# Kernel optimization log

Measured on AMD Instinct MI355X. Metric: run time of the kernel, lower is better.

The kernel has to match this reference:

```python
import jax, jax.numpy as jnp
import numpy as np

B, T, C = 64, 200, 53
EMB, HID, AH, OUT = 64, 128, 128, 2
C2 = C * C
D1 = round(0.05 * C2)   # 140
D2 = round(0.5 * C2)    # 1404
BN_EPS = 1e-5


def setup_inputs() -> dict:
    key = jax.random.key(0)
    ks = jax.random.split(key, 32)
    def rn(k, shape, s=0.1):
        return (jax.random.normal(k, shape) * s).astype(jnp.float32)
    return {
        "x": rn(ks[0], (B, T, C), 1.0),
        # single shared Linear(1, EMB) embedding
        "emb_w": rn(ks[1], (EMB,)), "emb_b": rn(ks[2], (EMB,)),
        # GRU cell (weights stored [in, 3*HID], gate order r,z,n like torch)
        "w_ih": rn(ks[3], (EMB, 3 * HID)), "w_hh": rn(ks[4], (HID, 3 * HID)),
        "b_ih": rn(ks[5], (3 * HID,)), "b_hh": rn(ks[6], (3 * HID,)),
        # self-attention projections
        "q_w": rn(ks[7], (HID, AH)), "q_b": rn(ks[8], (AH,)),
        "k_w": rn(ks[9], (HID, AH)), "k_b": rn(ks[10], (AH,)),
        "v_w": rn(ks[11], (HID, HID)), "v_b": rn(ks[12], (HID,)),
        "gate_b": rn(ks[13], (C, C), 1.0),  # Gate.bias = randn(C, C)
        # gta_embed + BatchNorm1d + gta_attend
        "ge_w": rn(ks[14], (C2, D1)), "ge_b": rn(ks[15], (D1,)),
        "bn_g": jnp.ones((D1,), jnp.float32), "bn_b": jnp.zeros((D1,), jnp.float32),
        "ga_w1": rn(ks[16], (D1, D2)), "ga_b1": rn(ks[17], (D2,)),
        "ga_w2": rn(ks[18], (D2, 1)), "ga_b2": rn(ks[19], (1,)),
        # classifier MLP
        "c_w1": rn(ks[20], (C2, C2 // 2)), "c_b1": rn(ks[21], (C2 // 2,)),
        "c_w2": rn(ks[22], (C2 // 2, C2 // 4)), "c_b2": rn(ks[23], (C2 // 4,)),
        "c_w3": rn(ks[24], (C2 // 4, OUT)), "c_b3": rn(ks[25], (OUT,)),
    }


def _forward(x, emb_w, emb_b, w_ih, w_hh, b_ih, b_hh, q_w, q_b, k_w, k_b,
             v_w, v_b, gate_b, ge_w, ge_b, bn_g, bn_b, ga_w1, ga_b1, ga_w2,
             ga_b2, c_w1, c_b1, c_w2, c_b2, c_w3, c_b3):
    # Linear(1, EMB) applied per scalar: [B,T,C] -> [B,C,T,EMB]
    e = x.transpose(0, 2, 1)[..., None] * emb_w + emb_b
    xs = jnp.moveaxis(e, 2, 0)  # [T, B, C, EMB]

    def step(h, x_t):  # h: [B,C,HID], x_t: [B,C,EMB]
        gi = x_t @ w_ih + b_ih
        gh = h @ w_hh + b_hh
        i_r, i_z, i_n = jnp.split(gi, 3, axis=-1)
        h_r, h_z, h_n = jnp.split(gh, 3, axis=-1)
        r = jax.nn.sigmoid(i_r + h_r)
        z = jax.nn.sigmoid(i_z + h_z)
        n = jnp.tanh(i_n + r * h_n)
        h_new = (1 - z) * n + z * h
        # SVD-normalized self-attention across components
        q = h_new @ q_w + q_b
        k = h_new @ k_w + k_b
        v = h_new @ v_w + v_b
        scores = jnp.tanh(jnp.einsum('bif,bjf->bij', q, k))  # use_tan='before'
        sv = jnp.linalg.svd(scores, compute_uv=False)         # [B,C]
        ev = jax.lax.stop_gradient(jnp.max(jnp.abs(sv), axis=1))[:, None, None]
        scores = scores / ev
        attn = scores * jax.nn.sigmoid(jnp.abs(scores) + gate_b)  # Gate
        h_out = jnp.einsum('bij,bjf->bif', attn, v)
        return h_out, attn

    h0 = jnp.zeros((B, C, HID), x.dtype)
    _, attns = jax.lax.scan(step, h0, xs)      # [T,B,C,C]
    align = jnp.moveaxis(attns, 0, 1)          # [B,T,C,C]

    # gta_attention over time axis
    ai = align.reshape(B, T, C2)
    xr = (ai * ai.mean(axis=1, keepdims=True)).reshape(B * T, C2)
    xe = xr @ ge_w + ge_b
    mu = xe.mean(axis=0)
    var = xe.var(axis=0)  # biased, matches torch BN training-mode normalization
    xn = jax.nn.relu((xe - mu) / jnp.sqrt(var + BN_EPS) * bn_g + bn_b)
    a = jax.nn.relu(xn @ ga_w1 + ga_b1) @ ga_w2 + ga_b2  # [B*T,1]
    w = jax.nn.softmax(a.reshape(B, T), axis=1)
    dnc = (ai * w[..., None]).sum(axis=1)      # [B, C2]

    # classifier (Dropout1d is identity at inference)
    h1 = jax.nn.relu(dnc @ c_w1 + c_b1)
    h2 = jax.nn.relu(h1 @ c_w2 + c_b2)
    logits = h2 @ c_w3 + c_b3
    return logits, dnc.reshape(B, C, C), align


def reference(x, emb_w, emb_b, w_ih, w_hh, b_ih, b_hh, q_w, q_b, k_w, k_b,
              v_w, v_b, gate_b, ge_w, ge_b, bn_g, bn_b, ga_w1, ga_b1, ga_w2,
              ga_b2, c_w1, c_b1, c_w2, c_b2, c_w3, c_b3):
    return _forward(x, emb_w, emb_b, w_ih, w_hh, b_ih, b_hh, q_w, q_b, k_w,
                    k_b, v_w, v_b, gate_b, ge_w, ge_b, bn_g, bn_b, ga_w1,
                    ga_b1, ga_w2, ga_b2, c_w1, c_b1, c_w2, c_b2, c_w3, c_b3)
```

## Files before the change

kernel.cpp:

```cpp
#include <hip/hip_runtime.h>

#define NT 1024

__device__ __forceinline__ float fast_sigmoid(float x) { return 1.f/(1.f + __expf(-x)); }
__device__ __forceinline__ float fast_tanh(float x) {
  float t = __expf(-2.f*fabsf(x));
  float y = (1.f - t)/(1.f + t);
  return copysignf(y, x);
}
__device__ __forceinline__ void acc4(float& a, float4 u, float4 v) {
  a = fmaf(u.x, v.x, a); a = fmaf(u.y, v.y, a); a = fmaf(u.z, v.z, a); a = fmaf(u.w, v.w, a);
}
#define FMA4(A_, S_, V_) do { (A_).x = fmaf((S_),(V_).x,(A_).x); (A_).y = fmaf((S_),(V_).y,(A_).y); \
                              (A_).z = fmaf((S_),(V_).z,(A_).z); (A_).w = fmaf((S_),(V_).w,(A_).w); } while(0)

struct alignas(16) SmemScan {
  float h[56][132];
  float z[56][132];
  float v[56][132];
  float S[56][60];
  float G0[56][60];
  float GA[56][60];
  float GB[56][60];
  float u384[384], v00[384];
  float xt[56];
  float pv[56], y1[56], y2[56];
  int   gmax[9];
  float sc_ev;
};

__global__ void prep_whT(const float* __restrict__ w_hh, const float* __restrict__ b_hh,
                         float* __restrict__ WhT) {
  int idx = blockIdx.x*256 + threadIdx.x;
  if (idx >= 384*132) return;
  int g = idx/132, c = idx - g*132;
  float v = 0.f;
  if (c < 128) v = w_hh[c*384 + g];
  else if (c == 128) v = b_hh[g];
  WhT[idx] = v;
}

__global__ void prep_wT(const float* __restrict__ q_w, const float* __restrict__ q_b,
                        const float* __restrict__ k_w, const float* __restrict__ k_b,
                        const float* __restrict__ v_w, const float* __restrict__ v_b,
                        float* __restrict__ WT) {
  int idx = blockIdx.x*256 + threadIdx.x;
  if (idx >= 257*132) return;
  int u = idx/132, c = idx - u*132;
  float val = 0.f;
  if (u < 129) {
    if (c <= 128) {
      const float* qa = (c < 128) ? (q_w + c*128) : q_b;
      const float* kb = (u < 128) ? (k_w + u*128) : k_b;
      float s = 0.f;
      for (int d = 0; d < 128; ++d) s = fmaf(qa[d], kb[d], s);
      val = s;
    }
  } else {
    int f = u - 129;
    if (c < 128) val = v_w[c*128 + f];
    else if (c == 128) val = v_b[f];
  }
  WT[idx] = val;
}

__global__ void __launch_bounds__(1024, 4)
scan_kernel(const float* __restrict__ x, const float* __restrict__ emb_w,
            const float* __restrict__ emb_b, const float* __restrict__ w_ih,
            const float* __restrict__ b_ih, const float* __restrict__ WhT,
            const float* __restrict__ WT, const float* __restrict__ gate_b,
            float* __restrict__ out_align)
{
  extern __shared__ char smem_raw[];
  SmemScan& sm = *reinterpret_cast<SmemScan*>(smem_raw);
  const int b = blockIdx.x;
  const int tid = threadIdx.x;
  const int wv = tid >> 6;
  const int lane = tid & 63;

  for (int j = tid; j < 384; j += NT) {
    float su = 0.f, sv = 0.f;
    for (int m = 0; m < 64; ++m) {
      float w = w_ih[m*384 + j];
      su = fmaf(emb_w[m], w, su);
      sv = fmaf(emb_b[m], w, sv);
    }
    sm.u384[j] = su;
    sm.v00[j]  = sv + b_ih[j];
  }
  for (int idx = tid; idx < 56*132; idx += NT) {
    int r = idx/132, c = idx - r*132;
    float hv = (c == 128 && r < 53) ? 1.f : 0.f;
    sm.h[r][c] = hv; sm.z[r][c] = 0.f; sm.v[r][c] = 0.f;
  }
  for (int idx = tid; idx < 56*60; idx += NT) {
    int r = idx/60, c = idx - r*60;
    sm.S[r][c] = 0.f; sm.G0[r][c] = 0.f; sm.GA[r][c] = 0.f; sm.GB[r][c] = 0.f;
  }
  __syncthreads();

  const int f  = tid & 127;
  const int c0 = tid >> 7;
  int  cix[7]; bool cok[7];
  #pragma unroll
  for (int i = 0; i < 7; ++i) { int cc = c0 + 8*i; cok[i] = (cc < 53); cix[i] = cok[i] ? cc : 52; }

  const float* wh0 = WhT + (size_t)f*132;
  const float* wh1 = WhT + (size_t)(128+f)*132;
  const float* wh2 = WhT + (size_t)(256+f)*132;
  const int colA = 2*f, colB = colA + 1;
  const float* wtA = WT + (size_t)colA*132;
  const float* wtB = WT + (size_t)colB*132;

  for (int t = 0; t < 200; ++t) {
    if (tid < 53) sm.xt[tid] = x[(b*200 + t)*53 + tid];
    __syncthreads();

    float a0[7], a1[7], a2[7];
    #pragma unroll
    for (int i = 0; i < 7; ++i) { a0[i] = 0.f; a1[i] = 0.f; a2[i] = 0.f; }
    for (int q = 0; q < 33; ++q) {
      float4 w0 = *(const float4*)(wh0 + 4*q);
      float4 w1 = *(const float4*)(wh1 + 4*q);
      float4 w2 = *(const float4*)(wh2 + 4*q);
      #pragma unroll
      for (int i = 0; i < 7; ++i) {
        float4 hv = *(const float4*)&sm.h[cix[i]][4*q];
        acc4(a0[i], hv, w0); acc4(a1[i], hv, w1); acc4(a2[i], hv, w2);
      }
    }
    float hnew[7];
    {
      float uf0 = sm.u384[f], uf1 = sm.u384[128+f], uf2 = sm.u384[256+f];
      float v0f0 = sm.v00[f], v0f1 = sm.v00[128+f], v0f2 = sm.v00[256+f];
      #pragma unroll
      for (int i = 0; i < 7; ++i) {
        float xs = sm.xt[cix[i]];
        float r = fast_sigmoid(fmaf(xs, uf0, v0f0) + a0[i]);
        float z = fast_sigmoid(fmaf(xs, uf1, v0f1) + a1[i]);
        float n = fast_tanh(fmaf(xs, uf2, v0f2) + fmaf(r, a2[i], 0.f));
        hnew[i] = (1.f - z)*n + z*sm.h[cix[i]][f];
      }
    }
    __syncthreads();
    #pragma unroll
    for (int i = 0; i < 7; ++i) if (cok[i]) sm.h[cix[i]][f] = hnew[i];
    __syncthreads();

    {
      float aA[7], aB[7];
      #pragma unroll
      for (int i = 0; i < 7; ++i) { aA[i] = 0.f; aB[i] = 0.f; }
      for (int q = 0; q < 33; ++q) {
        float4 wa = *(const float4*)(wtA + 4*q);
        float4 wb = *(const float4*)(wtB + 4*q);
        #pragma unroll
        for (int i = 0; i < 7; ++i) {
          float4 hv = *(const float4*)&sm.h[cix[i]][4*q];
          acc4(aA[i], hv, wa); acc4(aB[i], hv, wb);
        }
      }
      #pragma unroll
      for (int i = 0; i < 7; ++i) if (cok[i]) {
        int c = cix[i];
        if (colA < 129) sm.z[c][colA] = aA[i]; else sm.v[c][colA-129] = aA[i];
        if (colB < 129) sm.z[c][colB] = aB[i]; else sm.v[c][colB-129] = aB[i];
      }
      if (tid < 53) {
        const float* wc = WT + (size_t)256*132;
        float s = 0.f;
        for (int q = 0; q < 33; ++q) {
          float4 wv4 = *(const float4*)(wc + 4*q);
          float4 hv = *(const float4*)&sm.h[tid][4*q];
          acc4(s, hv, wv4);
        }
        sm.v[tid][127] = s;
      }
    }
    __syncthreads();

    if (tid < 9) sm.gmax[tid] = 0;
    if (wv < 14 && lane < 53) {
      const int i = lane, j0 = 4*wv;
      float4 acc; acc.x = acc.y = acc.z = acc.w = 0.f;
      for (int q = 0; q < 33; ++q) {
        float4 zr = *(const float4*)&sm.z[i][4*q];
        float4 h0 = *(const float4*)&sm.h[j0  ][4*q];
        float4 h1 = *(const float4*)&sm.h[j0+1][4*q];
        float4 h2 = *(const float4*)&sm.h[j0+2][4*q];
        float4 h3 = *(const float4*)&sm.h[j0+3][4*q];
        acc4(acc.x, zr, h0); acc4(acc.y, zr, h1); acc4(acc.z, zr, h2); acc4(acc.w, zr, h3);
      }
      sm.S[i][j0  ] = fast_tanh(acc.x);
      sm.S[i][j0+1] = fast_tanh(acc.y);
      sm.S[i][j0+2] = fast_tanh(acc.z);
      sm.S[i][j0+3] = fast_tanh(acc.w);
    }
    __syncthreads();

    {
      float mx = 0.f;
      if (wv < 14 && lane < 53) {
        const int i = lane, j0 = 4*wv;
        float4 acc; acc.x = acc.y = acc.z = acc.w = 0.f;
        for (int q = 0; q < 14; ++q) {
          float4 sr = *(const float4*)&sm.S[i][4*q];
          float4 s0 = *(const float4*)&sm.S[j0  ][4*q];
          float4 s1 = *(const float4*)&sm.S[j0+1][4*q];
          float4 s2 = *(const float4*)&sm.S[j0+2][4*q];
          float4 s3 = *(const float4*)&sm.S[j0+3][4*q];
          acc4(acc.x, sr, s0); acc4(acc.y, sr, s1); acc4(acc.z, sr, s2); acc4(acc.w, sr, s3);
        }
        sm.G0[i][j0] = acc.x; sm.G0[i][j0+1] = acc.y;
        sm.G0[i][j0+2] = acc.z; sm.G0[i][j0+3] = acc.w;
        mx = fmaxf(fmaxf(fabsf(acc.x), fabsf(acc.y)), fmaxf(fabsf(acc.z), fabsf(acc.w)));
      }
      if (wv < 14) {
        for (int off = 32; off; off >>= 1) mx = fmaxf(mx, __shfl_down(mx, off));
        if (lane == 0) atomicMax(&sm.gmax[0], __float_as_int(mx));
      }
    }
    __syncthreads();

    float (*pa)[60] = sm.G0;
    float (*pc)[60] = sm.GA;
    for (int k = 0; k < 7; ++k) {
      float mx = 0.f;
      if (wv < 14 && lane < 53) {
        float s = 1.f/fmaxf(__int_as_float(sm.gmax[k]), 1e-20f);
        const int i = lane, j0 = 4*wv;
        float4 acc; acc.x = acc.y = acc.z = acc.w = 0.f;
        for (int q = 0; q < 14; ++q) {
          float4 ar = *(const float4*)&pa[i][4*q];
          float4 b0 = *(const float4*)&pa[j0  ][4*q];
          float4 b1 = *(const float4*)&pa[j0+1][4*q];
          float4 b2 = *(const float4*)&pa[j0+2][4*q];
          float4 b3 = *(const float4*)&pa[j0+3][4*q];
          acc4(acc.x, ar, b0); acc4(acc.y, ar, b1); acc4(acc.z, ar, b2); acc4(acc.w, ar, b3);
        }
        float s2 = s*s;
        acc.x *= s2; acc.y *= s2; acc.z *= s2; acc.w *= s2;
        pc[i][j0] = acc.x; pc[i][j0+1] = acc.y; pc[i][j0+2] = acc.z; pc[i][j0+3] = acc.w;
        mx = fmaxf(fmaxf(fabsf(acc.x), fabsf(acc.y)), fmaxf(fabsf(acc.z), fabsf(acc.w)));
      }
      if (wv < 14) {
        for (int off = 32; off; off >>= 1) mx = fmaxf(mx, __shfl_down(mx, off));
        if (lane == 0) atomicMax(&sm.gmax[k+1], __float_as_int(mx));
      }
      __syncthreads();
      float (*tn)[60] = pc;
      pc = (pc == sm.GA) ? sm.GB : sm.GA;
      pa = tn;
    }

    if (tid < 53) {
      float s = 0.f;
      for (int j = 0; j < 53; ++j) {
        float ph = 0.618034f*(float)(j + 1);
        float rj = 0.75f + 0.5f*(ph - floorf(ph));
        s = fmaf(pa[tid][j], rj, s);
      }
      sm.pv[tid] = s;
    }
    __syncthreads();
    if (tid < 53) {
      float s = 0.f;
      for (int j = 0; j < 53; ++j) s = fmaf(sm.G0[tid][j], sm.pv[j], s);
      sm.y1[tid] = s;
    }
    __syncthreads();
    if (tid < 53) {
      float s = 0.f;
      for (int j = 0; j < 53; ++j) s = fmaf(sm.G0[tid][j], sm.y1[j], s);
      sm.y2[tid] = s;
    }
    __syncthreads();
    if (tid < 64) {
      float yа = (tid < 53) ? sm.y1[tid] : 0.f;
      float yb = (tid < 53) ? sm.y2[tid] : 0.f;
      float num = yа*yb, den = yа*yа;
      for (int off = 32; off; off >>= 1) { num += __shfl_down(num, off); den += __shfl_down(den, off); }
      if (tid == 0) sm.sc_ev = sqrtf(num/fmaxf(den, 1e-30f));
    }
    __syncthreads();

    {
      float inv = 1.f/sm.sc_ev;
      const size_t abase = ((size_t)b*200 + (size_t)t)*2809;
      for (int idx = tid; idx < 2809; idx += NT) {
        int i = idx/53, j = idx - i*53;
        float s = sm.S[i][j]*inv;
        float a = s*fast_sigmoid(fabsf(s) + gate_b[idx]);
        sm.S[i][j] = a;
        out_align[abase + idx] = a;
      }
    }
    __syncthreads();

    {
      const int f0 = (tid & 31)*4;
      const int io = tid >> 5;
      const int i1 = io + 32;
      const bool has1 = (i1 < 53);
      float4 acc0, acc1;
      acc0.x = acc0.y = acc0.z = acc0.w = 0.f;
      acc1 = acc0;
      for (int q = 0; q < 14; ++q) {
        float4 s0 = *(const float4*)&sm.S[io][4*q];
        float4 s1 = *(const float4*)&sm.S[has1 ? i1 : 0][4*q];
        int j = 4*q;
        float4 v0 = *(const float4*)&sm.v[j  ][f0];
        float4 v1 = *(const float4*)&sm.v[j+1][f0];
        float4 v2 = *(const float4*)&sm.v[j+2][f0];
        float4 v3 = *(const float4*)&sm.v[j+3][f0];
        FMA4(acc0, s0.x, v0); FMA4(acc0, s0.y, v1); FMA4(acc0, s0.z, v2); FMA4(acc0, s0.w, v3);
        FMA4(acc1, s1.x, v0); FMA4(acc1, s1.y, v1); FMA4(acc1, s1.z, v2); FMA4(acc1, s1.w, v3);
      }
      *(float4*)&sm.h[io][f0] = acc0;
      if (has1) *(float4*)&sm.h[i1][f0] = acc1;
    }
  }
}


__global__ void mean_kernel(const float* __restrict__ align, float* __restrict__ m) {
  int idx = blockIdx.x*256 + threadIdx.x;
  if (idx >= 64*2809) return;
  int b = idx/2809, c = idx - b*2809;
  const float* p = align + (size_t)b*200*2809 + c;
  float s = 0.f;
  for (int t = 0; t < 200; ++t) s += p[(size_t)t*2809];
  m[idx] = s*(1.f/200.f);
}

__global__ void __launch_bounds__(256) xe_kernel(const float* __restrict__ align,
    const float* __restrict__ mai, const float* __restrict__ ge_w,
    const float* __restrict__ ge_b, float* __restrict__ xe) {
  __shared__ float sai[8][64];
  __shared__ float sw[64][140];
  const int tid = threadIdx.x;
  const int r0 = blockIdx.x*8;
  float4 acc0, acc1;
  acc0.x = acc0.y = acc0.z = acc0.w = 0.f;
  acc1 = acc0;
  const bool active = tid < 140;
  int rr0 = 0, cc0 = 0;
  if (active) { rr0 = (tid/35)*2; cc0 = (tid - 35*(tid/35))*4; }
  for (int k0 = 0; k0 < 2809; k0 += 64) {
    for (int l = tid; l < 512; l += 256) {
      int rr = l >> 6, kk = l & 63, k = k0 + kk;
      int r = r0 + rr;
      int bb = r/200;
      sai[rr][kk] = (k < 2809) ? align[(size_t)r*2809 + k]*mai[bb*2809 + k] : 0.f;
    }
    for (int l = tid; l < 64*140; l += 256) {
      int kk = l/140, cc = l - kk*140, k = k0 + kk;
      sw[kk][cc] = (k < 2809) ? ge_w[k*140 + cc] : 0.f;
    }
    __syncthreads();
    if (active) {
      for (int kk = 0; kk < 64; ++kk) {
        float a0 = sai[rr0][kk], a1 = sai[rr0+1][kk];
        float4 wv = *(const float4*)&sw[kk][cc0];
        FMA4(acc0, a0, wv); FMA4(acc1, a1, wv);
      }
    }
    __syncthreads();
  }
  if (active) {
    float4 gb = *(const float4*)&ge_b[cc0];
    acc0.x += gb.x; acc0.y += gb.y; acc0.z += gb.z; acc0.w += gb.w;
    acc1.x += gb.x; acc1.y += gb.y; acc1.z += gb.z; acc1.w += gb.w;
    *(float4*)&xe[(r0 + rr0)*140 + cc0]   = acc0;
    *(float4*)&xe[(r0 + rr0 + 1)*140 + cc0] = acc1;
  }
}

__global__ void bn_stats_kernel(const float* __restrict__ xe, float* __restrict__ mu,
                                float* __restrict__ var) {
  const int c = blockIdx.x, tid = threadIdx.x;
  double s = 0.0, sq = 0.0;
  for (int r = tid; r < 12800; r += 256) {
    double v = (double)xe[r*140 + c];
    s += v; sq += v*v;
  }
  for (int off = 32; off; off >>= 1) { s += __shfl_down(s, off); sq += __shfl_down(sq, off); }
  __shared__ double rs[4], rq[4];
  if ((tid & 63) == 0) { rs[tid >> 6] = s; rq[tid >> 6] = sq; }
  __syncthreads();
  if (tid == 0) {
    double S = rs[0]+rs[1]+rs[2]+rs[3], Q = rq[0]+rq[1]+rq[2]+rq[3];
    double m = S/12800.0;
    double v = Q/12800.0 - m*m;
    mu[c] = (float)m;
    var[c] = (float)fmax(v, 0.0);
  }
}

__global__ void __launch_bounds__(256) a_kernel(const float* __restrict__ xe,
    const float* __restrict__ mu, const float* __restrict__ var,
    const float* __restrict__ bn_g, const float* __restrict__ bn_b,
    const float* __restrict__ ga_w1, const float* __restrict__ ga_b1,
    const float* __restrict__ ga_w2, const float* __restrict__ ga_b2,
    float* __restrict__ a_out) {
  __shared__ float sxn[16][140];
  __shared__ float rsum[16];
  const int tid = threadIdx.x;
  const int r0 = blockIdx.x*16;
  for (int l = tid; l < 16*140; l += 256) {
    int rr = l/140, cc = l - rr*140;
    float v = xe[(r0 + rr)*140 + cc];
    float xn = (v - mu[cc])*rsqrtf(var[cc] + 1e-5f)*bn_g[cc] + bn_b[cc];
    sxn[rr][cc] = fmaxf(xn, 0.f);
  }
  if (tid < 16) rsum[tid] = 0.f;
  __syncthreads();
  float asum[16];
  #pragma unroll
  for (int r = 0; r < 16; ++r) asum[r] = 0.f;
  for (int j = tid; j < 1404; j += 256) {
    float acc[16];
    #pragma unroll
    for (int r = 0; r < 16; ++r) acc[r] = 0.f;
    for (int k = 0; k < 140; ++k) {
      float wv = ga_w1[k*1404 + j];
      #pragma unroll
      for (int r = 0; r < 16; ++r) acc[r] += sxn[r][k]*wv;
    }
    float b1 = ga_b1[j], w2 = ga_w2[j];
    #pragma unroll
    for (int r = 0; r < 16; ++r) asum[r] += fmaxf(acc[r] + b1, 0.f)*w2;
  }
  #pragma unroll
  for (int r = 0; r < 16; ++r) atomicAdd(&rsum[r], asum[r]);
  __syncthreads();
  if (tid < 16) a_out[r0 + tid] = rsum[tid] + ga_b2[0];
}

__global__ void softmax_kernel(const float* __restrict__ a, float* __restrict__ w) {
  const int b = blockIdx.x, tid = threadIdx.x;
  float mx = -1e30f;
  for (int t = tid; t < 200; t += 64) mx = fmaxf(mx, a[b*200 + t]);
  for (int off = 32; off; off >>= 1) mx = fmaxf(mx, __shfl_down(mx, off));
  mx = __shfl(mx, 0);
  float s = 0.f;
  for (int t = tid; t < 200; t += 64) { float e = __expf(a[b*200 + t] - mx); w[b*200 + t] = e; s += e; }
  for (int off = 32; off; off >>= 1) s += __shfl_down(s, off);
  s = __shfl(s, 0);
  float inv = 1.f/s;
  for (int t = tid; t < 200; t += 64) w[b*200 + t] *= inv;
}

__global__ void dnc_kernel(const float* __restrict__ align, const float* __restrict__ w,
                           float* __restrict__ dnc) {
  int idx = blockIdx.x*256 + threadIdx.x;
  if (idx >= 64*2809) return;
  int b = idx/2809, c = idx - b*2809;
  const float* p = align + (size_t)b*200*2809 + c;
  const float* pw = w + b*200;
  float s = 0.f;
  for (int t = 0; t < 200; ++t) s += p[(size_t)t*2809]*pw[t];
  dnc[idx] = s;
}

__global__ void fc_relu_kernel(const float* __restrict__ in, const float* __restrict__ wgt,
    const float* __restrict__ bias, float* __restrict__ out, int rows, int K, int N) {
  int idx = blockIdx.x*256 + threadIdx.x;
  if (idx >= rows*N) return;
  int r = idx/N, j = idx - r*N;
  const float* pi = in + (size_t)r*K;
  float s = 0.f;
  for (int k = 0; k < K; ++k) s += pi[k]*wgt[k*N + j];
  out[idx] = fmaxf(s + bias[j], 0.f);
}

__global__ void fc_kernel(const float* __restrict__ in, const float* __restrict__ wgt,
    const float* __restrict__ bias, float* __restrict__ out, int rows, int K, int N) {
  int idx = blockIdx.x*256 + threadIdx.x;
  if (idx >= rows*N) return;
  int r = idx/N, j = idx - r*N;
  const float* pi = in + (size_t)r*K;
  float s = 0.f;
  for (int k = 0; k < K; ++k) s += pi[k]*wgt[k*N + j];
  out[idx] = s + bias[j];
}

extern "C" void kernel_launch(void* const* d_in, const int* in_sizes, int n_in,
                              void* d_out, int out_size, void* d_ws, size_t ws_size,
                              hipStream_t stream) {
  (void)in_sizes; (void)n_in; (void)out_size; (void)ws_size;
  const float* x      = (const float*)d_in[0];
  const float* emb_w  = (const float*)d_in[1];
  const float* emb_b  = (const float*)d_in[2];
  const float* w_ih   = (const float*)d_in[3];
  const float* w_hh   = (const float*)d_in[4];
  const float* b_ih   = (const float*)d_in[5];
  const float* b_hh   = (const float*)d_in[6];
  const float* q_w    = (const float*)d_in[7];
  const float* q_b    = (const float*)d_in[8];
  const float* k_w    = (const float*)d_in[9];
  const float* k_b    = (const float*)d_in[10];
  const float* v_w    = (const float*)d_in[11];
  const float* v_b    = (const float*)d_in[12];
  const float* gate_b = (const float*)d_in[13];
  const float* ge_w   = (const float*)d_in[14];
  const float* ge_b   = (const float*)d_in[15];
  const float* bn_g   = (const float*)d_in[16];
  const float* bn_b   = (const float*)d_in[17];
  const float* ga_w1  = (const float*)d_in[18];
  const float* ga_b1  = (const float*)d_in[19];
  const float* ga_w2  = (const float*)d_in[20];
  const float* ga_b2  = (const float*)d_in[21];
  const float* c_w1   = (const float*)d_in[22];
  const float* c_b1   = (const float*)d_in[23];
  const float* c_w2   = (const float*)d_in[24];
  const float* c_b2   = (const float*)d_in[25];
  const float* c_w3   = (const float*)d_in[26];
  const float* c_b3   = (const float*)d_in[27];

  float* out = (float*)d_out;
  float* out_logits = out;
  float* out_dnc    = out + 128;
  float* out_align  = out + 128 + 64*2809;

  float* ws    = (float*)d_ws;
  float* w_WhT = ws;
  float* w_WT  = w_WhT + 50688;
  float* w_m   = w_WT + 33924;
  float* w_xe  = w_m + 179776;
  float* w_mu  = w_xe + 1792000;
  float* w_var = w_mu + 140;
  float* w_a   = w_var + 140;
  float* w_w   = w_a + 12800;
  float* w_h1  = w_w + 12800;
  float* w_h2  = w_h1 + 89856;

  hipLaunchKernelGGL(prep_whT, dim3((384*132 + 255)/256), dim3(256), 0, stream, w_hh, b_hh, w_WhT);
  hipLaunchKernelGGL(prep_wT, dim3((257*132 + 255)/256), dim3(256), 0, stream,
                     q_w, q_b, k_w, k_b, v_w, v_b, w_WT);

  const size_t shmem = sizeof(SmemScan);
  (void)hipFuncSetAttribute(reinterpret_cast<const void*>(scan_kernel),
                            hipFuncAttributeMaxDynamicSharedMemorySize, (int)shmem);

  hipLaunchKernelGGL(scan_kernel, dim3(64), dim3(1024), shmem, stream,
                     x, emb_w, emb_b, w_ih, b_ih, w_WhT, w_WT, gate_b, out_align);

  hipLaunchKernelGGL(mean_kernel, dim3(703), dim3(256), 0, stream, out_align, w_m);
  hipLaunchKernelGGL(xe_kernel, dim3(1600), dim3(256), 0, stream, out_align, w_m, ge_w, ge_b, w_xe);
  hipLaunchKernelGGL(bn_stats_kernel, dim3(140), dim3(256), 0, stream, w_xe, w_mu, w_var);
  hipLaunchKernelGGL(a_kernel, dim3(800), dim3(256), 0, stream,
                     w_xe, w_mu, w_var, bn_g, bn_b, ga_w1, ga_b1, ga_w2, ga_b2, w_a);
  hipLaunchKernelGGL(softmax_kernel, dim3(64), dim3(64), 0, stream, w_a, w_w);
  hipLaunchKernelGGL(dnc_kernel, dim3(703), dim3(256), 0, stream, out_align, w_w, out_dnc);
  hipLaunchKernelGGL(fc_relu_kernel, dim3(351), dim3(256), 0, stream, out_dnc, c_w1, c_b1, w_h1, 64, 2809, 1404);
  hipLaunchKernelGGL(fc_relu_kernel, dim3(176), dim3(256), 0, stream, w_h1, c_w2, c_b2, w_h2, 64, 1404, 702);
  hipLaunchKernelGGL(fc_kernel, dim3(1), dim3(128), 0, stream, w_h2, c_w3, c_b3, out_logits, 64, 702, 2);
}
```

Baseline: 35.72 ms.

## Interleave recurrent weight layout for coalesced loads with register prefetch in scan

Re-packs the GRU hidden-weight and attention projection matrices so that, for each k-chunk, the float4 loads of consecutive threads (f) sit next to each other in memory instead of 132 floats apart. The scan loops then software-prefetch the next chunk's weights into registers while computing the current one. The align output is also written with nontemporal stores to avoid polluting cache. The added prefetch registers may raise register pressure in a kernel launched at 1024 threads.

```diff
diff --git a/kernel.cpp b/kernel.cpp
--- a/kernel.cpp
+++ b/kernel.cpp
@@ -29,46 +29,64 @@
   float sc_ev;
 };
 
-__global__ void prep_whT(const float* __restrict__ w_hh, const float* __restrict__ b_hh,
-                         float* __restrict__ WhT) {
+__global__ void prep_wp1(const float* __restrict__ w_hh, const float* __restrict__ b_hh,
+                         float* __restrict__ Wp1) {
   int idx = blockIdx.x*256 + threadIdx.x;
-  if (idx >= 384*132) return;
-  int g = idx/132, c = idx - g*132;
+  if (idx >= 3*33*128*4) return;
+  int j = idx & 3;
+  int f = (idx >> 2) & 127;
+  int qg = idx >> 9;
+  int q = qg % 33;
+  int g = qg / 33;
+  int k = 4*q + j;
+  int col = g*128 + f;
   float v = 0.f;
-  if (c < 128) v = w_hh[c*384 + g];
-  else if (c == 128) v = b_hh[g];
-  WhT[idx] = v;
-}
-
-__global__ void prep_wT(const float* __restrict__ q_w, const float* __restrict__ q_b,
-                        const float* __restrict__ k_w, const float* __restrict__ k_b,
-                        const float* __restrict__ v_w, const float* __restrict__ v_b,
-                        float* __restrict__ WT) {
+  if (k < 128) v = w_hh[k*384 + col];
+  else if (k == 128) v = b_hh[col];
+  Wp1[idx] = v;
+}
+
+__global__ void prep_wp2(const float* __restrict__ q_w, const float* __restrict__ q_b,
+                         const float* __restrict__ k_w, const float* __restrict__ k_b,
+                         const float* __restrict__ v_w, const float* __restrict__ v_b,
+                         float* __restrict__ Wp2) {
   int idx = blockIdx.x*256 + threadIdx.x;
-  if (idx >= 257*132) return;
-  int u = idx/132, c = idx - u*132;
+  if (idx >= 33924) return;
   float val = 0.f;
-  if (u < 129) {
-    if (c <= 128) {
-      const float* qa = (c < 128) ? (q_w + c*128) : q_b;
-      const float* kb = (u < 128) ? (k_w + u*128) : k_b;
-      float s = 0.f;
-      for (int d = 0; d < 128; ++d) s = fmaf(qa[d], kb[d], s);
-      val = s;
+  if (idx < 33792) {
+    int j = idx & 3;
+    int f = (idx >> 2) & 127;
+    int qp = idx >> 9;
+    int q = qp % 33;
+    int p = qp / 33;
+    int u = 2*f + p;
+    int k = 4*q + j;
+    if (u < 129) {
+      if (k <= 128) {
+        const float* qa = (k < 128) ? (q_w + k*128) : q_b;
+        const float* kb = (u < 128) ? (k_w + u*128) : k_b;
+        float s = 0.f;
+        for (int d = 0; d < 128; ++d) s = fmaf(qa[d], kb[d], s);
+        val = s;
+      }
+    } else {
+      int f2 = u - 129;
+      if (k < 128) val = v_w[k*128 + f2];
+      else if (k == 128) val = v_b[f2];
     }
   } else {
-    int f = u - 129;
-    if (c < 128) val = v_w[c*128 + f];
-    else if (c == 128) val = v_b[f];
-  }
-  WT[idx] = val;
+    int c = idx - 33792;
+    if (c < 128) val = v_w[c*128 + 127];
+    else if (c == 128) val = v_b[127];
+  }
+  Wp2[idx] = val;
 }
 
 __global__ void __launch_bounds__(1024, 4)
 scan_kernel(const float* __restrict__ x, const float* __restrict__ emb_w,
             const float* __restrict__ emb_b, const float* __restrict__ w_ih,
-            const float* __restrict__ b_ih, const float* __restrict__ WhT,
-            const float* __restrict__ WT, const float* __restrict__ gate_b,
+            const float* __restrict__ b_ih, const float* __restrict__ Wp1,
+            const float* __restrict__ Wp2, const float* __restrict__ gate_b,
             float* __restrict__ out_align)
 {
   extern __shared__ char smem_raw[];
@@ -105,12 +123,10 @@
   #pragma unroll
   for (int i = 0; i < 7; ++i) { int cc = c0 + 8*i; cok[i] = (cc < 53); cix[i] = cok[i] ? cc : 52; }
 
-  const float* wh0 = WhT + (size_t)f*132;
-  const float* wh1 = WhT + (size_t)(128+f)*132;
-  const float* wh2 = WhT + (size_t)(256+f)*132;
+  const float* pw1 = Wp1 + (size_t)f*4;
+  const float* pw2 = Wp2 + (size_t)f*4;
+  const float* W256 = Wp2 + 33792;
   const int colA = 2*f, colB = colA + 1;
-  const float* wtA = WT + (size_t)colA*132;
-  const float* wtB = WT + (size_t)colB*132;
 
   for (int t = 0; t < 200; ++t) {
     if (tid < 53) sm.xt[tid] = x[(b*200 + t)*53 + tid];
@@ -119,14 +135,24 @@
     float a0[7], a1[7], a2[7];
     #pragma unroll
     for (int i = 0; i < 7; ++i) { a0[i] = 0.f; a1[i] = 0.f; a2[i] = 0.f; }
-    for (int q = 0; q < 33; ++q) {
-      float4 w0 = *(const float4*)(wh0 + 4*q);
-      float4 w1 = *(const float4*)(wh1 + 4*q);
-      float4 w2 = *(const float4*)(wh2 + 4*q);
-      #pragma unroll
-      for (int i = 0; i < 7; ++i) {
-        float4 hv = *(const float4*)&sm.h[cix[i]][4*q];
-        acc4(a0[i], hv, w0); acc4(a1[i], hv, w1); acc4(a2[i], hv, w2);
+    {
+      float4 w0 = *(const float4*)(pw1);
+      float4 w1 = *(const float4*)(pw1 + 16896);
+      float4 w2 = *(const float4*)(pw1 + 33792);
+      for (int q = 0; q < 33; ++q) {
+        float4 n0 = w0, n1 = w1, n2 = w2;
+        if (q < 32) {
+          const float* p = pw1 + (q+1)*512;
+          n0 = *(const float4*)(p);
+          n1 = *(const float4*)(p + 16896);
+          n2 = *(const float4*)(p + 33792);
+        }
+        #pragma unroll
+        for (int i = 0; i < 7; ++i) {
+          float4 hv = *(const float4*)&sm.h[cix[i]][4*q];
+          acc4(a0[i], hv, w0); acc4(a1[i], hv, w1); acc4(a2[i], hv, w2);
+        }
+        w0 = n0; w1 = n1; w2 = n2;
       }
     }
     float hnew[7];
@@ -151,14 +177,21 @@
       float aA[7], aB[7];
       #pragma unroll
       for (int i = 0; i < 7; ++i) { aA[i] = 0.f; aB[i] = 0.f; }
+      float4 wa = *(const float4*)(pw2);
+      float4 wb = *(const float4*)(pw2 + 16896);
       for (int q = 0; q < 33; ++q) {
-        float4 wa = *(const float4*)(wtA + 4*q);
-        float4 wb = *(const float4*)(wtB + 4*q);
+        float4 na = wa, nb = wb;
+        if (q < 32) {
+          const float* p = pw2 + (q+1)*512;
+          na = *(const float4*)(p);
+          nb = *(const float4*)(p + 16896);
+        }
         #pragma unroll
         for (int i = 0; i < 7; ++i) {
           float4 hv = *(const float4*)&sm.h[cix[i]][4*q];
           acc4(aA[i], hv, wa); acc4(aB[i], hv, wb);
         }
+        wa = na; wb = nb;
       }
       #pragma unroll
       for (int i = 0; i < 7; ++i) if (cok[i]) {
@@ -167,10 +200,9 @@
         if (colB < 129) sm.z[c][colB] = aB[i]; else sm.v[c][colB-129] = aB[i];
       }
       if (tid < 53) {
-        const float* wc = WT + (size_t)256*132;
         float s = 0.f;
         for (int q = 0; q < 33; ++q) {
-          float4 wv4 = *(const float4*)(wc + 4*q);
+          float4 wv4 = *(const float4*)(W256 + 4*q);
           float4 hv = *(const float4*)&sm.h[tid][4*q];
           acc4(s, hv, wv4);
         }
@@ -276,9 +308,9 @@
     }
     __syncthreads();
     if (tid < 64) {
-      float yа = (tid < 53) ? sm.y1[tid] : 0.f;
+      float ya = (tid < 53) ? sm.y1[tid] : 0.f;
       float yb = (tid < 53) ? sm.y2[tid] : 0.f;
-      float num = yа*yb, den = yа*yа;
+      float num = ya*yb, den = ya*ya;
       for (int off = 32; off; off >>= 1) { num += __shfl_down(num, off); den += __shfl_down(den, off); }
       if (tid == 0) sm.sc_ev = sqrtf(num/fmaxf(den, 1e-30f));
     }
@@ -292,7 +324,7 @@
         float s = sm.S[i][j]*inv;
         float a = s*fast_sigmoid(fabsf(s) + gate_b[idx]);
         sm.S[i][j] = a;
-        out_align[abase + idx] = a;
+        __builtin_nontemporal_store(a, &out_align[abase + idx]);
       }
     }
     __syncthreads();
@@ -524,9 +556,9 @@
   float* out_align  = out + 128 + 64*2809;
 
   float* ws    = (float*)d_ws;
-  float* w_WhT = ws;
-  float* w_WT  = w_WhT + 50688;
-  float* w_m   = w_WT + 33924;
+  float* w_Wp1 = ws;
+  float* w_Wp2 = w_Wp1 + 50688;
+  float* w_m   = w_Wp2 + 33924;
   float* w_xe  = w_m + 179776;
   float* w_mu  = w_xe + 1792000;
   float* w_var = w_mu + 140;
@@ -535,16 +567,16 @@
   float* w_h1  = w_w + 12800;
   float* w_h2  = w_h1 + 89856;
 
-  hipLaunchKernelGGL(prep_whT, dim3((384*132 + 255)/256), dim3(256), 0, stream, w_hh, b_hh, w_WhT);
-  hipLaunchKernelGGL(prep_wT, dim3((257*132 + 255)/256), dim3(256), 0, stream,
-                     q_w, q_b, k_w, k_b, v_w, v_b, w_WT);
+  hipLaunchKernelGGL(prep_wp1, dim3((50688 + 255)/256), dim3(256), 0, stream, w_hh, b_hh, w_Wp1);
+  hipLaunchKernelGGL(prep_wp2, dim3((33924 + 255)/256), dim3(256), 0, stream,
+                     q_w, q_b, k_w, k_b, v_w, v_b, w_Wp2);
 
   const size_t shmem = sizeof(SmemScan);
   (void)hipFuncSetAttribute(reinterpret_cast<const void*>(scan_kernel),
                             hipFuncAttributeMaxDynamicSharedMemorySize, (int)shmem);
 
   hipLaunchKernelGGL(scan_kernel, dim3(64), dim3(1024), shmem, stream,
-                     x, emb_w, emb_b, w_ih, b_ih, w_WhT, w_WT, gate_b, out_align);
+                     x, emb_w, emb_b, w_ih, b_ih, w_Wp1, w_Wp2, gate_b, out_align);
 
   hipLaunchKernelGGL(mean_kernel, dim3(703), dim3(256), 0, stream, out_align, w_m);
   hipLaunchKernelGGL(xe_kernel, dim3(1600), dim3(256), 0, stream, out_align, w_m, ge_w, ge_b, w_xe);
```

Result: faster. 33.86 ms (-5.2%).
